# Kernel tuning notes

Measured on AMD Instinct MI355X. Metric: run time of the kernel, lower is better.

Reference implementation:

```python
import jax, jax.numpy as jnp
import numpy as np

T, B, D_IN, D_H = 512, 64, 1024, 1024


def setup_inputs() -> dict:
    key = jax.random.key(0)
    ks = jax.random.split(key, 11)
    s = 1.0 / np.sqrt(D_H)
    u = lambda k, shape: jax.random.uniform(k, shape, jnp.float32, -s, s)
    return {
        "emb": jax.random.normal(ks[0], (T, B, D_IN), jnp.float32),
        "hx": jax.random.normal(ks[1], (1, B, D_H), jnp.float32),
        "w_ih_u": u(ks[2], (D_H, D_IN)),
        "w_ih_r": u(ks[3], (D_H, D_IN)),
        "w_ih_c": u(ks[4], (D_H, D_IN)),
        "w_hh_u": u(ks[5], (D_H, D_H)),
        "w_hh_r": u(ks[6], (D_H, D_H)),
        "w_hh_c": u(ks[7], (D_H, D_H)),
        "b_u": u(ks[8], (D_H,)),
        "b_r": u(ks[9], (D_H,)),
        "b_c": u(ks[10], (D_H,)),
    }


def reference(emb, hx, w_ih_u, w_ih_r, w_ih_c, w_hh_u, w_hh_r, w_hh_c, b_u, b_r, b_c):
    # Eval-mode BayesGRU: weight-noise diffs are zero, plain GRU-style recurrence.
    def step(h, x):            # h: [1,B,H], x: [B,D_IN]
        h0 = h[0]              # [B,H]
        upd = jax.nn.sigmoid(x @ w_ih_u.T + h0 @ w_hh_u.T + b_u)
        rst = jax.nn.sigmoid(x @ w_ih_r.T + h0 @ w_hh_r.T + b_r)
        cel = jnp.tanh(x @ w_ih_c.T + (rst * h0) @ w_hh_c.T + b_c)
        hy = (1.0 - upd) * h + upd * cel   # broadcasts to [1,B,H]
        return hy, hy

    hx_final, outs = jax.lax.scan(step, hx, emb)
    outputs = outs.reshape(T, B, D_H)      # torch.cat along dim 0; squeeze(1) no-op for B>1
    return outputs, hx_final
```

## Files before the change

### kernel.cpp

```cpp
#include <hip/hip_runtime.h>
#include <hip/hip_bf16.h>
#include <stdint.h>


#define T_STEPS 512
#define BATCH   64
#define DIN     1024
#define DH      1024
#define NWG     128
#define SLAB    65536

typedef __attribute__((ext_vector_type(8))) short bf16x8;
typedef __attribute__((ext_vector_type(4))) float f32x4;

static __device__ __forceinline__ unsigned short f2bf(float x) {
    union { float f; uint32_t u; } v; v.f = x;
    uint32_t u = v.u;
    return (unsigned short)((u + 0x7FFFu + ((u >> 16) & 1u)) >> 16);
}
static __device__ __forceinline__ float bf2f(unsigned short u) {
    union { uint32_t v; float f; } x; x.v = (uint32_t)u << 16; return x.f;
}
static __device__ __forceinline__ bf16x8 cvt8(float4 a, float4 b) {
    union { bf16x8 v; unsigned d[4]; } u;
    asm("v_cvt_pk_bf16_f32 %0, %1, %2" : "=v"(u.d[0]) : "v"(a.x), "v"(a.y));
    asm("v_cvt_pk_bf16_f32 %0, %1, %2" : "=v"(u.d[1]) : "v"(a.z), "v"(a.w));
    asm("v_cvt_pk_bf16_f32 %0, %1, %2" : "=v"(u.d[2]) : "v"(b.x), "v"(b.y));
    asm("v_cvt_pk_bf16_f32 %0, %1, %2" : "=v"(u.d[3]) : "v"(b.z), "v"(b.w));
    return u.v;
}

static __device__ __forceinline__ int fidx(int row, int k) {
    return ((((row >> 4) * 32 + (k >> 5)) * 64) + (((k >> 3) & 3) * 16) + (row & 15)) * 8
           + (k & 7);
}

static __device__ __forceinline__ void st_wt_u16(void* p, unsigned v) {
    asm volatile("global_store_short %0, %1, off sc0 sc1" :: "v"(p), "v"(v) : "memory");
}
static __device__ __forceinline__ bf16x8 ld_llc(const unsigned short* p) {
    bf16x8 r;
    asm volatile("global_load_dwordx4 %0, %1, off sc0 sc1" : "=v"(r) : "v"(p));
    return r;
}
static __device__ __forceinline__ unsigned ld_llc_u16(const unsigned short* p) {
    unsigned r;
    asm volatile("global_load_ushort %0, %1, off sc0 sc1" : "=v"(r) : "v"(p));
    return r;
}
static __device__ __forceinline__ void vwait0() {
    asm volatile("s_waitcnt vmcnt(0)" ::: "memory");
    __builtin_amdgcn_sched_barrier(0);
}

static __device__ __forceinline__ void wait_fam(const int* cnt, int t, int fam, int quota) {
    const int* b = cnt + t * 128 + fam;
    for (;;) {
        int a0,a1,a2,a3,a4,a5,a6,a7;
        asm volatile("global_load_dword %0, %1, off sc0 sc1" : "=v"(a0) : "v"(b));
        asm volatile("global_load_dword %0, %1, off sc0 sc1" : "=v"(a1) : "v"(b+16));
        asm volatile("global_load_dword %0, %1, off sc0 sc1" : "=v"(a2) : "v"(b+32));
        asm volatile("global_load_dword %0, %1, off sc0 sc1" : "=v"(a3) : "v"(b+48));
        asm volatile("global_load_dword %0, %1, off sc0 sc1" : "=v"(a4) : "v"(b+64));
        asm volatile("global_load_dword %0, %1, off sc0 sc1" : "=v"(a5) : "v"(b+80));
        asm volatile("global_load_dword %0, %1, off sc0 sc1" : "=v"(a6) : "v"(b+96));
        asm volatile("global_load_dword %0, %1, off sc0 sc1" : "=v"(a7) : "v"(b+112));
        asm volatile("s_waitcnt vmcnt(0)" ::: "memory");
        __builtin_amdgcn_sched_barrier(0);
        if (a0>=quota && a1>=quota && a2>=quota && a3>=quota &&
            a4>=quota && a5>=quota && a6>=quota && a7>=quota) break;
        __builtin_amdgcn_s_sleep(2);
    }
}
static __device__ __forceinline__ void wg_wait(const int* cnt, int t, int fam, int quota) {
    if (threadIdx.x == 0) wait_fam(cnt, t, fam, quota);
    __syncthreads();
}
static __device__ __forceinline__ void post_fam(int* cnt, int t, int g, int fam) {
    __hip_atomic_fetch_add(cnt + t * 128 + g * 16 + fam, 1,
                           __ATOMIC_RELAXED, __HIP_MEMORY_SCOPE_AGENT);
}

__global__ __launch_bounds__(256) void gru_pack_weights(
    const float* __restrict__ wihu, const float* __restrict__ wihr,
    const float* __restrict__ wihc, const float* __restrict__ whhu,
    const float* __restrict__ whhr, const float* __restrict__ whhc,
    unsigned short* __restrict__ Wur, unsigned short* __restrict__ Wc)
{
    const int total = 3072 * 2048;
    for (int idx = blockIdx.x * 256 + threadIdx.x; idx < total; idx += gridDim.x * 256) {
        int n = idx >> 11;
        int k = idx & 2047;
        int j = n & 1023;
        float v;
        if (n < 1024)      v = (k < DIN) ? wihu[j*DIN + k] : whhu[j*DH + (k - DIN)];
        else if (n < 2048) v = (k < DIN) ? wihr[j*DIN + k] : whhr[j*DH + (k - DIN)];
        else               v = (k < DIN) ? wihc[j*DIN + k] : whhc[j*DH + (k - DIN)];
        unsigned short bv = f2bf(v);
        int kk = k >> 5, kg = (k >> 3) & 3, r = k & 7;
        if (n < 2048) {
            int b = n >> 4, col = n & 15;
            Wur[((((size_t)kk*128 + b)*4 + kg)*16 + col)*8 + r] = bv;
        } else {
            int nc = n - 2048, b = nc >> 4, col = nc & 15;
            Wc [((((size_t)kk*64 + b)*4 + kg)*16 + col)*8 + r] = bv;
        }
    }
}

__global__ __launch_bounds__(256) void gru_convert_x(
    const float* __restrict__ emb, unsigned short* __restrict__ xbf)
{
    size_t i = (size_t)blockIdx.x * 256 + threadIdx.x;
    float4 v = ((const float4*)emb)[i];
    ushort4 b;
    b.x = f2bf(v.x); b.y = f2bf(v.y); b.z = f2bf(v.z); b.w = f2bf(v.w);
    ((ushort4*)xbf)[i] = b;
}

__global__ __launch_bounds__(256) void gru_init(
    const float* __restrict__ hx, unsigned short* __restrict__ hA,
    int* __restrict__ cnt)
{
    int i = blockIdx.x * 256 + threadIdx.x;
    int row = i >> 10, k = i & 1023;
    hA[fidx(row, k)] = f2bf(hx[i]);
    cnt[i] = 0;
}

__global__ __launch_bounds__(256, 1) void gru_persistent(
    const unsigned short* __restrict__ Wur, const unsigned short* __restrict__ Wc,
    const float* __restrict__ emb, const unsigned short* __restrict__ xbf,
    const float* __restrict__ hx,
    const float* __restrict__ bu, const float* __restrict__ br, const float* __restrict__ bc,
    unsigned short* __restrict__ hA, unsigned short* __restrict__ rh,
    float* __restrict__ out, int* __restrict__ cnt, int deep)
{
    __shared__ unsigned short wur_s[32768];
    __shared__ unsigned short wc_s [32768];

    const int wg   = blockIdx.x;
    const int tid  = threadIdx.x;
    const int lane = tid & 63;
    const int wid  = tid >> 6;
    const int m0   = wid * 16;
    const int c15  = lane & 15;
    const int kg   = lane >> 4;

    for (int i = tid; i < 4096; i += 256) {
        int kk = i >> 6, j = i & 63;
        *((uint4*)wur_s + i) =
            *(const uint4*)((const char*)Wur + ((size_t)kk*128 + wg)*1024 + j*16);
    }
    if (wg < 64) {
        for (int i = tid; i < 4096; i += 256) {
            int kk = i >> 6, j = i & 63;
            *((uint4*)wc_s + i) =
                *(const uint4*)((const char*)Wc + ((size_t)kk*64 + wg)*1024 + j*16);
        }
    }
    __syncthreads();

    const int v    = wg & 63;
    const int colj = v * 16 + c15;

    if (wg < 64) {
        const float bu_ = bu[colj], bc_ = bc[colj];
        float hreg[4];
        #pragma unroll
        for (int i = 0; i < 4; ++i) hreg[i] = hx[(m0 + kg*4 + i) * DH + colj];

        for (int t = 0; t < T_STEPS; ++t) {
            const int par = t & 1;
            const unsigned short* ha   = hA + par * SLAB;
            unsigned short*       hnxt = hA + (par ^ 1) * SLAB;

            f32x4 au = {0.f,0.f,0.f,0.f}, ac = {0.f,0.f,0.f,0.f};
            bf16x8 fr[32];

            if (deep) {
                const unsigned short* xp =
                    xbf + ((size_t)t * BATCH + (m0 + c15)) * DIN + kg * 8;
                #pragma unroll
                for (int kk = 0; kk < 32; ++kk) {
                    bf16x8 f = *(const bf16x8*)(xp + kk * 32);
                    au = __builtin_amdgcn_mfma_f32_16x16x32_bf16(
                             f, *(const bf16x8*)(wur_s + kk*512 + lane*8), au, 0, 0, 0);
                    ac = __builtin_amdgcn_mfma_f32_16x16x32_bf16(
                             f, *(const bf16x8*)(wc_s + kk*512 + lane*8), ac, 0, 0, 0);
                }
            } else {
                const float* xp = emb + ((size_t)t * BATCH + (m0 + c15)) * DIN + kg * 8;
                #pragma unroll
                for (int kk = 0; kk < 32; ++kk) {
                    float4 a = *(const float4*)(xp + kk * 32);
                    float4 b = *(const float4*)(xp + kk * 32 + 4);
                    bf16x8 f = cvt8(a, b);
                    au = __builtin_amdgcn_mfma_f32_16x16x32_bf16(
                             f, *(const bf16x8*)(wur_s + kk*512 + lane*8), au, 0, 0, 0);
                    ac = __builtin_amdgcn_mfma_f32_16x16x32_bf16(
                             f, *(const bf16x8*)(wc_s + kk*512 + lane*8), ac, 0, 0, 0);
                }
            }

            if (t) wg_wait(cnt, t-1, 0, 8);
            const unsigned short* hb = ha + wid * 16384;
            #pragma unroll
            for (int kk = 0; kk < 32; ++kk) fr[kk] = ld_llc(hb + kk * 512 + lane * 8);
            vwait0();
            #pragma unroll
            for (int kk = 0; kk < 32; ++kk)
                au = __builtin_amdgcn_mfma_f32_16x16x32_bf16(
                         fr[kk], *(const bf16x8*)(wur_s + (kk+32)*512 + lane*8), au, 0, 0, 0);
            float ureg[4];
            #pragma unroll
            for (int i = 0; i < 4; ++i)
                ureg[i] = 1.f / (1.f + __expf(-(au[i] + bu_)));

            const unsigned short* rb = rh + wid * 16384;
            wg_wait(cnt, t, 1, 4);
            #pragma unroll
            for (int kk = 0; kk < 16; ++kk) fr[kk] = ld_llc(rb + kk * 512 + lane * 8);
            vwait0();
            #pragma unroll
            for (int kk = 0; kk < 16; ++kk)
                ac = __builtin_amdgcn_mfma_f32_16x16x32_bf16(
                         fr[kk], *(const bf16x8*)(wc_s + (kk+32)*512 + lane*8), ac, 0, 0, 0);
            wg_wait(cnt, t, 2, 4);
            #pragma unroll
            for (int kk = 0; kk < 16; ++kk) fr[kk] = ld_llc(rb + (kk+16) * 512 + lane * 8);
            vwait0();
            #pragma unroll
            for (int kk = 0; kk < 16; ++kk)
                ac = __builtin_amdgcn_mfma_f32_16x16x32_bf16(
                         fr[kk], *(const bf16x8*)(wc_s + (kk+48)*512 + lane*8), ac, 0, 0, 0);

            float hnv[4];
            #pragma unroll
            for (int i = 0; i < 4; ++i) {
                int row = m0 + kg * 4 + i;
                float pre = ac[i] + bc_;
                float e   = __expf(2.f * pre);
                float cel = 1.f - 2.f / (e + 1.f);
                float hn  = (1.f - ureg[i]) * hreg[i] + ureg[i] * cel;
                hreg[i] = hn;
                hnv[i]  = hn;
                st_wt_u16(hnxt + fidx(row, colj), (unsigned)f2bf(hn));
            }
            asm volatile("s_waitcnt vmcnt(0)" ::: "memory");
            __syncthreads();
            if (tid == 0) post_fam(cnt, t, wg >> 3, 0);

            float* out_t = out + (size_t)t * SLAB;
            #pragma unroll
            for (int i = 0; i < 4; ++i) {
                int row = m0 + kg * 4 + i;
                out_t[row * DH + colj] = hnv[i];
                if (t == T_STEPS - 1)
                    out[(size_t)T_STEPS * SLAB + row * DH + colj] = hnv[i];
            }
        }
    } else {
        const float br_ = br[colj];
        for (int t = 0; t < T_STEPS; ++t) {
            const int par = t & 1;
            const unsigned short* ha = hA + par * SLAB;

            f32x4 ar = {0.f,0.f,0.f,0.f};
            bf16x8 fr[32];

            if (deep) {
                const unsigned short* xp =
                    xbf + ((size_t)t * BATCH + (m0 + c15)) * DIN + kg * 8;
                #pragma unroll
                for (int kk = 0; kk < 32; ++kk)
                    ar = __builtin_amdgcn_mfma_f32_16x16x32_bf16(
                             *(const bf16x8*)(xp + kk * 32),
                             *(const bf16x8*)(wur_s + kk*512 + lane*8), ar, 0, 0, 0);
            } else {
                const float* xp = emb + ((size_t)t * BATCH + (m0 + c15)) * DIN + kg * 8;
                #pragma unroll
                for (int kk = 0; kk < 32; ++kk) {
                    float4 a = *(const float4*)(xp + kk * 32);
                    float4 b = *(const float4*)(xp + kk * 32 + 4);
                    ar = __builtin_amdgcn_mfma_f32_16x16x32_bf16(
                             cvt8(a, b), *(const bf16x8*)(wur_s + kk*512 + lane*8),
                             ar, 0, 0, 0);
                }
            }

            if (t) wg_wait(cnt, t-1, 0, 8);
            const unsigned short* hb = ha + wid * 16384;
            unsigned hp16[4];
            #pragma unroll
            for (int i = 0; i < 4; ++i)
                hp16[i] = ld_llc_u16(ha + fidx(m0 + kg*4 + i, colj));
            #pragma unroll
            for (int kk = 0; kk < 32; ++kk) fr[kk] = ld_llc(hb + kk * 512 + lane * 8);
            vwait0();
            #pragma unroll
            for (int kk = 0; kk < 32; ++kk)
                ar = __builtin_amdgcn_mfma_f32_16x16x32_bf16(
                         fr[kk], *(const bf16x8*)(wur_s + (kk+32)*512 + lane*8),
                         ar, 0, 0, 0);

            #pragma unroll
            for (int i = 0; i < 4; ++i) {
                int row = m0 + kg * 4 + i;
                float s = 1.f / (1.f + __expf(-(ar[i] + br_)));
                st_wt_u16(rh + fidx(row, colj),
                          (unsigned)f2bf(s * bf2f((unsigned short)hp16[i])));
            }
            asm volatile("s_waitcnt vmcnt(0)" ::: "memory");
            __syncthreads();
            if (tid == 0) {
                if (v < 32) post_fam(cnt, t, v >> 2, 1);
                else        post_fam(cnt, t, (v - 32) >> 2, 2);
            }
        }
    }
}

extern "C" void kernel_launch(void* const* d_in, const int* in_sizes, int n_in,
                              void* d_out, int out_size, void* d_ws, size_t ws_size,
                              hipStream_t stream)
{
    const float* emb  = (const float*)d_in[0];
    const float* hx   = (const float*)d_in[1];
    const float* wihu = (const float*)d_in[2];
    const float* wihr = (const float*)d_in[3];
    const float* wihc = (const float*)d_in[4];
    const float* whhu = (const float*)d_in[5];
    const float* whhr = (const float*)d_in[6];
    const float* whhc = (const float*)d_in[7];
    const float* bu   = (const float*)d_in[8];
    const float* br   = (const float*)d_in[9];
    const float* bc   = (const float*)d_in[10];
    float* out = (float*)d_out;
    char*  ws  = (char*)d_ws;

    unsigned short* Wur = (unsigned short*)(ws + 0);
    unsigned short* Wc  = (unsigned short*)(ws + 8388608);
    int*            cnt = (int*)(ws + 12582912);
    unsigned short* hA  = (unsigned short*)(ws + 12845056);
    unsigned short* rhb = (unsigned short*)(ws + 13107200);
    unsigned short* xbf = (unsigned short*)(ws + 16777216);
    const int deep = (ws_size >= 83886080ull) ? 1 : 0;

    gru_pack_weights<<<1024, 256, 0, stream>>>(wihu, wihr, wihc, whhu, whhr, whhc, Wur, Wc);
    if (deep) gru_convert_x<<<32768, 256, 0, stream>>>(emb, xbf);
    gru_init<<<256, 256, 0, stream>>>(hx, hA, cnt);
    gru_persistent<<<NWG, 256, 0, stream>>>(Wur, Wc, emb, xbf, hx, bu, br, bc,
                                            hA, rhb, out, cnt, deep);
}
```

Baseline: 5.003 ms.

## Prefetch recurrent h/rh loads before x-projection and coalesce h stores via LDS bounce

Moves the wait on the previous step's h and the issue of its 32 fragment loads ahead of the input-projection MFMAs, so the LLC load latency overlaps with the x·W compute. The update-gate workgroups also issue the first rh half-load before the u-gate hidden MFMAs, using a separate fragment register array. Per-element 16-bit write-through stores of h and r*h are replaced by staging the values in a small LDS bounce buffer, then issuing one 64-bit store per lane into the fragment layout. This cuts the number of global store instructions on the critical cross-workgroup path, at the cost of more live VGPRs and an LDS round trip.

```diff
diff --git a/kernel.cpp b/kernel.cpp
--- a/kernel.cpp
+++ b/kernel.cpp
@@ -35,8 +35,8 @@
            + (k & 7);
 }
 
-static __device__ __forceinline__ void st_wt_u16(void* p, unsigned v) {
-    asm volatile("global_store_short %0, %1, off sc0 sc1" :: "v"(p), "v"(v) : "memory");
+static __device__ __forceinline__ void st_wt_u64(void* p, unsigned long long v) {
+    asm volatile("global_store_dwordx2 %0, %1, off sc0 sc1" :: "v"(p), "v"(v) : "memory");
 }
 static __device__ __forceinline__ bf16x8 ld_llc(const unsigned short* p) {
     bf16x8 r;
@@ -50,6 +50,10 @@
 }
 static __device__ __forceinline__ void vwait0() {
     asm volatile("s_waitcnt vmcnt(0)" ::: "memory");
+    __builtin_amdgcn_sched_barrier(0);
+}
+static __device__ __forceinline__ void lwait0() {
+    asm volatile("s_waitcnt lgkmcnt(0)" ::: "memory");
     __builtin_amdgcn_sched_barrier(0);
 }
 
@@ -138,6 +142,7 @@
 {
     __shared__ unsigned short wur_s[32768];
     __shared__ unsigned short wc_s [32768];
+    __shared__ __align__(8) unsigned short bounce[1024];
 
     const int wg   = blockIdx.x;
     const int tid  = threadIdx.x;
@@ -163,6 +168,9 @@
 
     const int v    = wg & 63;
     const int colj = v * 16 + c15;
+    const int regionBase = (wid * 32 + (v >> 1)) * 512 + (v & 1) * 256;
+    const int bpos = (c15 >> 3) * 128 + (c15 & 7);
+    unsigned short* bw = bounce + wid * 256;
 
     if (wg < 64) {
         const float bu_ = bu[colj], bc_ = bc[colj];
@@ -177,6 +185,12 @@
 
             f32x4 au = {0.f,0.f,0.f,0.f}, ac = {0.f,0.f,0.f,0.f};
             bf16x8 fr[32];
+            bf16x8 fr2[16];
+
+            if (t) wg_wait(cnt, t-1, 0, 8);
+            const unsigned short* hb = ha + wid * 16384;
+            #pragma unroll
+            for (int kk = 0; kk < 32; ++kk) fr[kk] = ld_llc(hb + kk * 512 + lane * 8);
 
             if (deep) {
                 const unsigned short* xp =
@@ -202,12 +216,13 @@
                              f, *(const bf16x8*)(wc_s + kk*512 + lane*8), ac, 0, 0, 0);
                 }
             }
-
-            if (t) wg_wait(cnt, t-1, 0, 8);
-            const unsigned short* hb = ha + wid * 16384;
-            #pragma unroll
-            for (int kk = 0; kk < 32; ++kk) fr[kk] = ld_llc(hb + kk * 512 + lane * 8);
             vwait0();
+
+            const unsigned short* rb = rh + wid * 16384;
+            wg_wait(cnt, t, 1, 4);
+            #pragma unroll
+            for (int kk = 0; kk < 16; ++kk) fr2[kk] = ld_llc(rb + kk * 512 + lane * 8);
+
             #pragma unroll
             for (int kk = 0; kk < 32; ++kk)
                 au = __builtin_amdgcn_mfma_f32_16x16x32_bf16(
@@ -217,35 +232,36 @@
             for (int i = 0; i < 4; ++i)
                 ureg[i] = 1.f / (1.f + __expf(-(au[i] + bu_)));
 
-            const unsigned short* rb = rh + wid * 16384;
-            wg_wait(cnt, t, 1, 4);
-            #pragma unroll
-            for (int kk = 0; kk < 16; ++kk) fr[kk] = ld_llc(rb + kk * 512 + lane * 8);
             vwait0();
             #pragma unroll
             for (int kk = 0; kk < 16; ++kk)
                 ac = __builtin_amdgcn_mfma_f32_16x16x32_bf16(
-                         fr[kk], *(const bf16x8*)(wc_s + (kk+32)*512 + lane*8), ac, 0, 0, 0);
+                         fr2[kk], *(const bf16x8*)(wc_s + (kk+32)*512 + lane*8), ac, 0, 0, 0);
+
             wg_wait(cnt, t, 2, 4);
             #pragma unroll
-            for (int kk = 0; kk < 16; ++kk) fr[kk] = ld_llc(rb + (kk+16) * 512 + lane * 8);
+            for (int kk = 0; kk < 16; ++kk) fr2[kk] = ld_llc(rb + (kk+16) * 512 + lane * 8);
             vwait0();
             #pragma unroll
             for (int kk = 0; kk < 16; ++kk)
                 ac = __builtin_amdgcn_mfma_f32_16x16x32_bf16(
-                         fr[kk], *(const bf16x8*)(wc_s + (kk+48)*512 + lane*8), ac, 0, 0, 0);
+                         fr2[kk], *(const bf16x8*)(wc_s + (kk+48)*512 + lane*8), ac, 0, 0, 0);
 
             float hnv[4];
             #pragma unroll
             for (int i = 0; i < 4; ++i) {
-                int row = m0 + kg * 4 + i;
                 float pre = ac[i] + bc_;
                 float e   = __expf(2.f * pre);
                 float cel = 1.f - 2.f / (e + 1.f);
                 float hn  = (1.f - ureg[i]) * hreg[i] + ureg[i] * cel;
                 hreg[i] = hn;
                 hnv[i]  = hn;
-                st_wt_u16(hnxt + fidx(row, colj), (unsigned)f2bf(hn));
+                bw[bpos + (kg * 4 + i) * 8] = f2bf(hn);
+            }
+            lwait0();
+            {
+                unsigned long long pk = *(const unsigned long long*)(bw + lane * 4);
+                st_wt_u64(hnxt + regionBase + lane * 4, pk);
             }
             asm volatile("s_waitcnt vmcnt(0)" ::: "memory");
             __syncthreads();
@@ -268,6 +284,15 @@
 
             f32x4 ar = {0.f,0.f,0.f,0.f};
             bf16x8 fr[32];
+
+            if (t) wg_wait(cnt, t-1, 0, 8);
+            const unsigned short* hb = ha + wid * 16384;
+            unsigned hp16[4];
+            #pragma unroll
+            for (int i = 0; i < 4; ++i)
+                hp16[i] = ld_llc_u16(ha + fidx(m0 + kg*4 + i, colj));
+            #pragma unroll
+            for (int kk = 0; kk < 32; ++kk) fr[kk] = ld_llc(hb + kk * 512 + lane * 8);
 
             if (deep) {
                 const unsigned short* xp =
@@ -288,16 +313,8 @@
                              ar, 0, 0, 0);
                 }
             }
-
-            if (t) wg_wait(cnt, t-1, 0, 8);
-            const unsigned short* hb = ha + wid * 16384;
-            unsigned hp16[4];
-            #pragma unroll
-            for (int i = 0; i < 4; ++i)
-                hp16[i] = ld_llc_u16(ha + fidx(m0 + kg*4 + i, colj));
-            #pragma unroll
-            for (int kk = 0; kk < 32; ++kk) fr[kk] = ld_llc(hb + kk * 512 + lane * 8);
             vwait0();
+
             #pragma unroll
             for (int kk = 0; kk < 32; ++kk)
                 ar = __builtin_amdgcn_mfma_f32_16x16x32_bf16(
@@ -306,10 +323,14 @@
 
             #pragma unroll
             for (int i = 0; i < 4; ++i) {
-                int row = m0 + kg * 4 + i;
                 float s = 1.f / (1.f + __expf(-(ar[i] + br_)));
-                st_wt_u16(rh + fidx(row, colj),
-                          (unsigned)f2bf(s * bf2f((unsigned short)hp16[i])));
+                bw[bpos + (kg * 4 + i) * 8] =
+                    f2bf(s * bf2f((unsigned short)hp16[i]));
+            }
+            lwait0();
+            {
+                unsigned long long pk = *(const unsigned long long*)(bw + lane * 4);
+                st_wt_u64(rh + regionBase + lane * 4, pk);
             }
             asm volatile("s_waitcnt vmcnt(0)" ::: "memory");
             __syncthreads();
```

New measurement: 7.280 ms. +45.5%, slower.
